# Kernel tuning notes

Hardware: AMD Instinct MI355X
Metric: run time of the kernel (lower is better)

## Reference

```python
import jax, jax.numpy as jnp
import numpy as np

PDIM = 64
SK = 3
LK = 13

def setup_inputs() -> dict:
    key = jax.random.key(0)
    ks = jax.random.split(key, 6)
    B, C, H, W = 16, 128, 64, 64
    x = jax.random.normal(ks[0], (B, C, H, W), dtype=jnp.float32)
    lk_filter = jax.random.normal(ks[1], (PDIM, PDIM, LK, LK), dtype=jnp.float32) * 0.02
    w1 = jax.random.normal(ks[2], (PDIM // 2, PDIM), dtype=jnp.float32) * 0.1
    b1 = jax.random.normal(ks[3], (PDIM // 2,), dtype=jnp.float32) * 0.1
    w2 = jax.random.normal(ks[4], (PDIM * SK * SK, PDIM // 2), dtype=jnp.float32) * 0.1
    b2 = jax.random.normal(ks[5], (PDIM * SK * SK,), dtype=jnp.float32) * 0.1
    return {"x": x, "lk_filter": lk_filter, "w1": w1, "b1": b1, "w2": w2, "b2": b2}

def reference(x, lk_filter, w1, b1, w2, b2):
    B, C, H, W = x.shape
    x1, x2 = x[:, :PDIM], x[:, PDIM:]

    # dwc_proj: global avg pool -> 1x1 conv -> GELU -> 1x1 conv (per-sample 3x3 kernels)
    pooled = jnp.mean(x[:, :PDIM], axis=(2, 3))                     # [B, pdim]
    h = jax.nn.gelu(pooled @ w1.T + b1, approximate=False)          # [B, pdim//2]
    dyn = (h @ w2.T + b2).reshape(B, PDIM, SK * SK)                 # [B, pdim, 9]

    # dynamic depthwise 3x3 conv, per (batch, channel) kernel, padding=1
    pad = SK // 2
    xp = jnp.pad(x1, ((0, 0), (0, 0), (pad, pad), (pad, pad)))
    patches = jnp.stack([xp[:, :, i:i + H, j:j + W]
                         for i in range(SK) for j in range(SK)], axis=2)  # [B, pdim, 9, H, W]
    x1_dyn = jnp.einsum('bckhw,bck->bchw', patches, dyn)

    # large-kernel dense conv, padding = LK//2 (SAME for odd LK)
    p = LK // 2
    x1_lk = jax.lax.conv_general_dilated(
        x1, lk_filter, window_strides=(1, 1), padding=[(p, p), (p, p)],
        dimension_numbers=('NCHW', 'OIHW', 'NCHW'))

    x1_out = x1_lk + x1_dyn
    return jnp.concatenate([x1_out, x2], axis=1)
```

## Files before the change

kernel.cpp:

```cpp
#include <hip/hip_runtime.h>
#include <hip/hip_bf16.h>

typedef short  short8  __attribute__((ext_vector_type(8)));
typedef float  f32x16  __attribute__((ext_vector_type(16)));

#define XB 16
#define XC 128
#define XH 64
#define XW 64
#define XHW 4096
#define PSTR 72
#define XPROW 76

__device__ __forceinline__ unsigned short f2bf(float f) {
    union { float f; unsigned int u; } v; v.f = f;
    unsigned int r = (v.u + 0x7fffu + ((v.u >> 16) & 1u)) >> 16;
    return (unsigned short)r;
}

__global__ void k_prep(const float* __restrict__ x, unsigned short* __restrict__ xpad,
                       float* __restrict__ rs,
                       const float* __restrict__ lk, unsigned short* __restrict__ fpack) {
    int blk = blockIdx.x;
    int t = threadIdx.x;
    if (blk >= 1216) {
        int tidx = (blk - 1216) * 256 + t;
        int l   = tidx & 63;
        int g   = (tidx >> 6) & 1;
        int ks  = (tidx >> 7) & 3;
        int tap = tidx >> 9;
        int oc  = g * 32 + (l & 31);
        int ic0 = ks * 16 + (l >> 5) * 8;
        unsigned short tmp[8];
#pragma unroll
        for (int e = 0; e < 8; ++e)
            tmp[e] = f2bf(lk[(size_t)(oc * 64 + ic0 + e) * 169 + tap]);
        unsigned int u[4];
#pragma unroll
        for (int k = 0; k < 4; ++k) u[k] = (unsigned int)tmp[2 * k] | ((unsigned int)tmp[2 * k + 1] << 16);
        uint4 v = {u[0], u[1], u[2], u[3]};
        *(uint4*)(fpack + (size_t)tidx * 8) = v;
        return;
    }
    int b = blk / 76, hp = blk - b * 76;
    unsigned short* dst = xpad + (size_t)(b * XPROW + hp) * XPROW * PSTR;
    uint4 z = {0u, 0u, 0u, 0u};
    if (hp < 6 || hp >= 70) {
        for (int k = t; k < 684; k += 256) ((uint4*)dst)[k] = z;
        return;
    }
    int h = hp - 6;
    __shared__ float tile[64][65];
    __shared__ float ps[4][64];
    {
        int w = t & 63, cg = t >> 6;
#pragma unroll
        for (int k = 0; k < 16; ++k) {
            int c = cg * 16 + k;
            tile[c][w] = x[(size_t)b * XC * XHW + (size_t)c * XHW + h * 64 + w];
        }
    }
    __syncthreads();
    {
        int c = t & 63, q = t >> 6;
        float s = 0.f;
#pragma unroll
        for (int k = 0; k < 16; ++k) s += tile[c][q * 16 + k];
        ps[q][c] = s;
    }
    __syncthreads();
    if (t < 64) {
        float tot = ps[0][t] + ps[1][t] + ps[2][t] + ps[3][t];
        rs[b * 4096 + h * 64 + t] = tot * (1.f / 4096.f);
    }
    if (t < 108) {
        int px = t / 9, u = t - (t / 9) * 9;
        int ppx = px < 6 ? px : px + 64;
        ((uint4*)(dst + ppx * PSTR))[u] = z;
    }
    {
        int px = t >> 2, cp = t & 3;
        unsigned short tmp[16];
#pragma unroll
        for (int k = 0; k < 16; ++k) tmp[k] = f2bf(tile[cp * 16 + k][px]);
        unsigned int u[8];
#pragma unroll
        for (int k = 0; k < 8; ++k) u[k] = (unsigned int)tmp[2 * k] | ((unsigned int)tmp[2 * k + 1] << 16);
        uint4 v0 = {u[0], u[1], u[2], u[3]};
        uint4 v1 = {u[4], u[5], u[6], u[7]};
        unsigned short* dp = dst + (px + 6) * PSTR + cp * 16;
        *(uint4*)dp = v0;
        *((uint4*)dp + 1) = v1;
        if (cp == 0) ((uint4*)(dst + (px + 6) * PSTR))[8] = z;
    }
}

__global__ __launch_bounds__(512, 2) void k_conv(const unsigned short* __restrict__ xpad,
                                                 const unsigned short* __restrict__ fpack,
                                                 const float* __restrict__ rs,
                                                 const float* __restrict__ w1, const float* __restrict__ b1,
                                                 const float* __restrict__ w2, const float* __restrict__ b2,
                                                 const float* __restrict__ x,
                                                 float* __restrict__ out) {
    extern __shared__ unsigned short lds[];
    unsigned short* ldsDyn = lds + 56448;
    float* ldsH = (float*)(lds + 57024);
    float* ldsP = (float*)(lds + 57088);
    int blk = blockIdx.x;
    int b = blk >> 4, tile = blk & 15;
    int th = tile >> 2, tw = tile & 3;
    int Y0 = th * 16, X0 = tw * 16;
    int t = threadIdx.x;

    if (t < 64) {
        const float* rp = rs + b * 4096 + t;
        float s = 0.f;
#pragma unroll
        for (int h = 0; h < 64; ++h) s += rp[h * 64];
        ldsP[t] = s;
        if (t < 32) {
            float s1 = b1[t];
#pragma unroll
            for (int c = 0; c < 64; ++c) s1 += ldsP[c] * w1[t * 64 + c];
            ldsH[t] = 0.5f * s1 * (1.f + erff(s1 * 0.70710678118654752f));
        }
    }

    {
        const unsigned short* srcb = xpad + ((size_t)(b * XPROW + Y0) * XPROW + X0) * PSTR;
        for (int k = t; k < 7056; k += 512) {
            int r = k / 252, o = k - r * 252;
            *(uint4*)(lds + r * 28 * PSTR + o * 8) =
                *(const uint4*)(srcb + (size_t)r * XPROW * PSTR + o * 8);
        }
    }
    __syncthreads();

    {
        float s = b2[t];
#pragma unroll
        for (int i = 0; i < 32; ++i) s += ldsH[i] * w2[t * 32 + i];
        ldsDyn[t] = f2bf(s);
        if (t < 64) {
            int o2 = 512 + t;
            float s2 = b2[o2];
#pragma unroll
            for (int i = 0; i < 32; ++i) s2 += ldsH[i] * w2[o2 * 32 + i];
            ldsDyn[o2] = f2bf(s2);
        }
    }
    __syncthreads();

    int wave = t >> 6, l = t & 63;
    int ks = wave & 3, fc = wave >> 2;
    int l31 = l & 31, lhi = l >> 5;

    int abase = ((l31 >> 3) * 28 + fc * 8 + (l31 & 7)) * PSTR + lhi * 8 + ks * 16;

    f32x16 acc[4][2];
#pragma unroll
    for (int m = 0; m < 4; ++m)
#pragma unroll
        for (int n = 0; n < 2; ++n)
#pragma unroll
            for (int r = 0; r < 16; ++r) acc[m][n][r] = 0.f;

    const unsigned short* fb = fpack + ks * 1024 + l * 8;

#pragma unroll 1
    for (int i = 0; i < 13; ++i) {
        const unsigned short* brow = fb + (size_t)(i * 13) * 4096;
        int arow = abase + i * 28 * PSTR;
#pragma unroll
        for (int j = 0; j < 13; ++j) {
            short8 b0 = *(const short8*)(brow + j * 4096);
            short8 b1v = *(const short8*)(brow + j * 4096 + 512);
            int aoff = arow + j * PSTR;
            __builtin_amdgcn_s_setprio(1);
#pragma unroll
            for (int fr = 0; fr < 4; ++fr) {
                short8 a = *(const short8*)(lds + aoff + fr * 8064);
                acc[fr][0] = __builtin_amdgcn_mfma_f32_32x32x16_bf16(a, b0, acc[fr][0], 0, 0, 0);
                acc[fr][1] = __builtin_amdgcn_mfma_f32_32x32x16_bf16(a, b1v, acc[fr][1], 0, 0, 0);
            }
            __builtin_amdgcn_s_setprio(0);
        }
    }

    {
        int ebase = ks * 16 + lhi * 8;
        int e0 = l31 - ebase;
        int e1 = 32 + l31 - ebase;
#pragma unroll
        for (int di = 0; di < 3; ++di)
#pragma unroll
            for (int dj = 0; dj < 3; ++dj) {
                int tp = di * 3 + dj;
                unsigned short v0 = ldsDyn[l31 * 9 + tp];
                unsigned short v1 = ldsDyn[(32 + l31) * 9 + tp];
                short8 b0, b1v;
#pragma unroll
                for (int s = 0; s < 8; ++s) {
                    b0[s] = (s == e0) ? (short)v0 : (short)0;
                    b1v[s] = (s == e1) ? (short)v1 : (short)0;
                }
                int aoff = abase + ((di + 5) * 28 + (dj + 5)) * PSTR;
#pragma unroll
                for (int fr = 0; fr < 4; ++fr) {
                    short8 a = *(const short8*)(lds + aoff + fr * 8064);
                    acc[fr][0] = __builtin_amdgcn_mfma_f32_32x32x16_bf16(a, b0, acc[fr][0], 0, 0, 0);
                    acc[fr][1] = __builtin_amdgcn_mfma_f32_32x32x16_bf16(a, b1v, acc[fr][1], 0, 0, 0);
                }
            }
    }
    __syncthreads();

    float* lf = (float*)lds;
#pragma unroll
    for (int fr = 0; fr < 4; ++fr) {
#pragma unroll
        for (int n = 0; n < 2; ++n)
#pragma unroll
            for (int r = 0; r < 16; ++r) {
                int oc = n * 32 + l31;
                int px = (r >> 2) * 16 + fc * 8 + (r & 3) + 4 * lhi;
                lf[ks * 4160 + oc * 65 + px] = acc[fr][n][r];
            }
        __syncthreads();
#pragma unroll
        for (int k2 = 0; k2 < 8; ++k2) {
            int e = k2 * 512 + t;
            int oc = e >> 6, px = e & 63;
            int idx = oc * 65 + px;
            float s = lf[idx] + lf[4160 + idx] + lf[8320 + idx] + lf[12480 + idx];
            int y = Y0 + fr * 4 + (px >> 4);
            int xx = X0 + (px & 15);
            out[((size_t)(b * XC + oc) * XH + y) * XW + xx] = s;
        }
        __syncthreads();
    }

    {
        const uint4* xs = (const uint4*)x;
        uint4* od = (uint4*)out;
#pragma unroll
        for (int q = 0; q < 8; ++q) {
            int m4 = blk * 4096 + q * 512 + t;
            int bi = m4 >> 16;
            int rem = m4 & 65535;
            size_t off = (size_t)bi * 131072 + 65536 + rem;
            od[off] = xs[off];
        }
    }
}

extern "C" void kernel_launch(void* const* d_in, const int* in_sizes, int n_in,
                              void* d_out, int out_size, void* d_ws, size_t ws_size,
                              hipStream_t stream) {
    const float* x  = (const float*)d_in[0];
    const float* lk = (const float*)d_in[1];
    const float* w1 = (const float*)d_in[2];
    const float* b1 = (const float*)d_in[3];
    const float* w2 = (const float*)d_in[4];
    const float* b2 = (const float*)d_in[5];
    float* out = (float*)d_out;

    char* ws = (char*)d_ws;
    float*          rs     = (float*)ws;
    unsigned short* fpack  = (unsigned short*)(ws + 1048576);
    unsigned short* xpad   = (unsigned short*)(ws + 2605056);

    k_prep<<<1554, 256, 0, stream>>>(x, xpad, rs, lk, fpack);
    k_conv<<<256, 512, 114432, stream>>>(xpad, fpack, rs, w1, b1, w2, b2, x, out);
}
```

Baseline: 104.2 us.

## Stream filter fragments through a per-wave LDS double buffer with async global-to-LDS loads

Measured after the change: 103.3 us (median of 2 runs). No clear change (-0.8%).

```diff
diff --git a/kernel.cpp b/kernel.cpp
--- a/kernel.cpp
+++ b/kernel.cpp
@@ -16,6 +16,12 @@
     union { float f; unsigned int u; } v; v.f = f;
     unsigned int r = (v.u + 0x7fffu + ((v.u >> 16) & 1u)) >> 16;
     return (unsigned short)r;
+}
+
+__device__ __forceinline__ void gload16(const unsigned short* g, unsigned short* s) {
+    __builtin_amdgcn_global_load_lds(
+        (const __attribute__((address_space(1))) void*)g,
+        (__attribute__((address_space(3))) void*)s, 16, 0, 0);
 }
 
 __global__ void k_prep(const float* __restrict__ x, unsigned short* __restrict__ xpad,
@@ -103,14 +109,23 @@
                                                  const float* __restrict__ x,
                                                  float* __restrict__ out) {
     extern __shared__ unsigned short lds[];
-    unsigned short* ldsDyn = lds + 56448;
-    float* ldsH = (float*)(lds + 57024);
-    float* ldsP = (float*)(lds + 57088);
+    unsigned short* ldsDyn = lds + 72832;
+    float* ldsH = (float*)(lds + 73408);
+    float* ldsP = (float*)(lds + 73472);
     int blk = blockIdx.x;
     int b = blk >> 4, tile = blk & 15;
     int th = tile >> 2, tw = tile & 3;
     int Y0 = th * 16, X0 = tw * 16;
     int t = threadIdx.x;
+    int wave = t >> 6, l = t & 63;
+    int ks = wave & 3, fc = wave >> 2;
+    int l31 = l & 31, lhi = l >> 5;
+
+    unsigned short* bring = lds + 56448 + wave * 2048;
+    const unsigned short* gB = fpack + ks * 1024 + l * 8;
+
+    gload16(gB, bring);
+    gload16(gB + 512, bring + 512);
 
     if (t < 64) {
         const float* rp = rs + b * 4096 + t;
@@ -151,10 +166,6 @@
     }
     __syncthreads();
 
-    int wave = t >> 6, l = t & 63;
-    int ks = wave & 3, fc = wave >> 2;
-    int l31 = l & 31, lhi = l >> 5;
-
     int abase = ((l31 >> 3) * 28 + fc * 8 + (l31 & 7)) * PSTR + lhi * 8 + ks * 16;
 
     f32x16 acc[4][2];
@@ -165,26 +176,31 @@
 #pragma unroll
             for (int r = 0; r < 16; ++r) acc[m][n][r] = 0.f;
 
-    const unsigned short* fb = fpack + ks * 1024 + l * 8;
-
+    int ar = abase, jj = 0;
 #pragma unroll 1
-    for (int i = 0; i < 13; ++i) {
-        const unsigned short* brow = fb + (size_t)(i * 13) * 4096;
-        int arow = abase + i * 28 * PSTR;
-#pragma unroll
-        for (int j = 0; j < 13; ++j) {
-            short8 b0 = *(const short8*)(brow + j * 4096);
-            short8 b1v = *(const short8*)(brow + j * 4096 + 512);
-            int aoff = arow + j * PSTR;
-            __builtin_amdgcn_s_setprio(1);
-#pragma unroll
-            for (int fr = 0; fr < 4; ++fr) {
-                short8 a = *(const short8*)(lds + aoff + fr * 8064);
-                acc[fr][0] = __builtin_amdgcn_mfma_f32_32x32x16_bf16(a, b0, acc[fr][0], 0, 0, 0);
-                acc[fr][1] = __builtin_amdgcn_mfma_f32_32x32x16_bf16(a, b1v, acc[fr][1], 0, 0, 0);
-            }
-            __builtin_amdgcn_s_setprio(0);
-        }
+    for (int tt = 0; tt < 169; ++tt) {
+        if (tt < 168) {
+            const unsigned short* src = gB + (size_t)(tt + 1) * 4096;
+            unsigned short* dstp = bring + ((tt + 1) & 1) * 1024;
+            gload16(src, dstp);
+            gload16(src + 512, dstp + 512);
+            asm volatile("s_waitcnt vmcnt(2)" ::: "memory");
+        } else {
+            asm volatile("s_waitcnt vmcnt(0)" ::: "memory");
+        }
+        const unsigned short* bp = bring + (tt & 1) * 1024 + l * 8;
+        short8 b0  = *(const short8*)(bp);
+        short8 b1v = *(const short8*)(bp + 512);
+        __builtin_amdgcn_s_setprio(1);
+#pragma unroll
+        for (int fr = 0; fr < 4; ++fr) {
+            short8 a = *(const short8*)(lds + ar + fr * 8064);
+            acc[fr][0] = __builtin_amdgcn_mfma_f32_32x32x16_bf16(a, b0, acc[fr][0], 0, 0, 0);
+            acc[fr][1] = __builtin_amdgcn_mfma_f32_32x32x16_bf16(a, b1v, acc[fr][1], 0, 0, 0);
+        }
+        __builtin_amdgcn_s_setprio(0);
+        ++jj; ar += PSTR;
+        if (jj == 13) { jj = 0; ar += 15 * PSTR; }
     }
 
     {
@@ -271,5 +287,5 @@
     unsigned short* xpad   = (unsigned short*)(ws + 2605056);
 
     k_prep<<<1554, 256, 0, stream>>>(x, xpad, rs, lk, fpack);
-    k_conv<<<256, 512, 114432, stream>>>(xpad, fpack, rs, w1, b1, w2, b2, x, out);
-}
+    k_conv<<<256, 512, 147200, stream>>>(xpad, fpack, rs, w1, b1, w2, b2, x, out);
+}
```
